# Optimization experiments

Hardware: AMD Instinct MI355X
Metric: run time of the kernel (lower is better)

## Reference

```python
import jax, jax.numpy as jnp
import numpy as np

DIM = 8   # dim == degree, required for the pol[n] * kron_power broadcast to be valid
DEG = 8
NEU = 4


def setup_inputs() -> dict:
    key = jax.random.key(0)
    ks = jax.random.split(key, DEG + 2)
    inp = {
        "X": jax.random.uniform(ks[0], (NEU, DIM), dtype=jnp.float32),      # stacked neurons
        "bias": jax.random.uniform(ks[1], (DIM,), dtype=jnp.float32),       # pol[0] for each polynomial
    }
    for n in range(1, DEG + 1):
        # pol[n] for each of the DIM polynomials: (DIM, DIM**n)
        inp[f"c{n}"] = jax.random.uniform(ks[1 + n], (DIM, DIM ** n), dtype=jnp.float32)
    return inp


def reference(X, bias, c1, c2, c3, c4, c5, c6, c7, c8):
    # output[n_idx, p_idx] = bias[p_idx] + sum_{n=1..DEG} <c_n[p_idx], kron^n(x_{n_idx})>
    coefs = [c1, c2, c3, c4, c5, c6, c7, c8]
    N = X.shape[0]
    out = jnp.broadcast_to(bias[None, :], (N, bias.shape[0]))
    K = X  # Kronecker power 1 of each neuron, shape (N, DIM)
    for i, c in enumerate(coefs):
        out = out + K @ c.T  # (N, DIM**n) @ (DIM**n, DIM) -> (N, DIM)
        if i < len(coefs) - 1:
            # khart([x, K]) == kron(x, K) per row: result[i*len(K)+j] = x[i]*K[j]
            K = (X[:, :, None] * K[:, None, :]).reshape(N, -1)
    return out
```

## Files before the change

### kernel.cpp

```cpp
#include <hip/hip_runtime.h>
#include <hip/hip_bf16.h>
#include <stdint.h>

#define OFF7 32768
#define OFF6 36864
#define OFF5 37376
#define OFF4 37440
#define NSEG 37448
#define NQ   (NSEG * 4)

typedef __attribute__((address_space(1))) const uint32_t g_u32;
typedef __attribute__((address_space(3))) uint32_t l_u32;

__device__ __forceinline__ void gload_lds16(const float* g, float* l) {
    __builtin_amdgcn_global_load_lds((g_u32*)g, (l_u32*)l, 16, 0, 0);
}

__device__ __forceinline__ float4 mul4(float4 a, float4 b) {
    return make_float4(a.x * b.x, a.y * b.y, a.z * b.z, a.w * b.w);
}
__device__ __forceinline__ float4 fma4s(float s, float4 b, float4 c) {
    return make_float4(fmaf(s, b.x, c.x), fmaf(s, b.y, c.y),
                       fmaf(s, b.z, c.z), fmaf(s, b.w, c.w));
}
__device__ __forceinline__ float4 fma44(float4 a, float4 b, float4 c) {
    return make_float4(fmaf(a.x, b.x, c.x), fmaf(a.y, b.y, c.y),
                       fmaf(a.z, b.z, c.z), fmaf(a.w, b.w, c.w));
}

struct SegInfo {
    const float* seg;
    float4 th;
    int p;
};

__device__ __forceinline__ SegInfo seg_decode(
    int g,
    const float* c4, const float* c5, const float* c6,
    const float* c7, const float* c8,
    const float4* T1s, const float4* T2s)
{
    SegInfo si;
    if (g < OFF7) {
        si.p = g >> 12; int hi = g & 4095;
        si.seg = c8 + ((size_t)si.p << 24) + ((size_t)hi << 12);
        si.th = mul4(T2s[hi >> 6], T2s[hi & 63]);
    } else if (g < OFF6) {
        int t = g - OFF7; si.p = t >> 9; int hi = t & 511;
        si.seg = c7 + ((size_t)si.p << 21) + ((size_t)hi << 12);
        si.th = mul4(T1s[hi >> 6], T2s[hi & 63]);
    } else if (g < OFF5) {
        int t = g - OFF6; si.p = t >> 6; int hi = t & 63;
        si.seg = c6 + ((size_t)si.p << 18) + ((size_t)hi << 12);
        si.th = T2s[hi];
    } else if (g < OFF4) {
        int t = g - OFF5; si.p = t >> 3; int hi = t & 7;
        si.seg = c5 + ((size_t)si.p << 15) + ((size_t)hi << 12);
        si.th = T1s[hi];
    } else {
        si.p = g - OFF4;
        si.seg = c4 + ((size_t)si.p << 12);
        si.th = make_float4(1.f, 1.f, 1.f, 1.f);
    }
    return si;
}

#define STAGE(dst, segptr, u) { \
    _Pragma("unroll") \
    for (int j_ = 0; j_ < 4; ++j_) { \
        gload_lds16((segptr) + ((((u) << 2) + j_) << 8) + (lane << 2), \
                    (dst) + (j_ << 8)); \
    } }

__global__ __launch_bounds__(256) void poly_big(
    const float* __restrict__ X,
    const float* __restrict__ c4, const float* __restrict__ c5,
    const float* __restrict__ c6, const float* __restrict__ c7,
    const float* __restrict__ c8, float* __restrict__ ws)
{
    __shared__ float4 T1s[8], T2s[64];
    __shared__ float part[32];
    __shared__ float buf[2][4096];
    const int tid = threadIdx.x;

    if (tid < 8)  T1s[tid] = make_float4(X[tid], X[8 + tid], X[16 + tid], X[24 + tid]);
    if (tid < 32) part[tid] = 0.f;
    __syncthreads();
    if (tid < 64) T2s[tid] = mul4(T1s[tid >> 3], T1s[tid & 7]);
    __syncthreads();

    const int wave = tid >> 6;
    const int lane = tid & 63;
    const int lhi  = lane >> 4;
    const float4 tl0 = T2s[((lane & 15) << 2) + 0];
    const float4 tl1 = T2s[((lane & 15) << 2) + 1];
    const float4 tl2 = T2s[((lane & 15) << 2) + 2];
    const float4 tl3 = T2s[((lane & 15) << 2) + 3];

    const int wg = (blockIdx.x << 2) + wave;
    const int NW = gridDim.x << 2;
    int Q    = (int)(((long long)wg * NQ) / NW);
    int Qend = (int)(((long long)(wg + 1) * NQ) / NW);

    if (Q < Qend) {
        float* h0 = &buf[0][wave << 10];
        float* h1 = &buf[1][wave << 10];
        float* cbuf = h0;
        float* nbuf = h1;

        SegInfo cur = seg_decode(Q >> 2, c4, c5, c6, c7, c8, T1s, T2s);
        int curu = Q & 3;
        int curp = cur.p;
        STAGE(cbuf, cur.seg, curu);

        float4 runacc = make_float4(0.f, 0.f, 0.f, 0.f);
        for (;;) {
            const bool more = (Q + 1) < Qend;
            SegInfo nxt = cur;
            int nxtu = curu;
            if (more) {
                nxtu = (Q + 1) & 3;
                nxt = seg_decode((Q + 1) >> 2, c4, c5, c6, c7, c8, T1s, T2s);
                STAGE(nbuf, nxt.seg, nxtu);
                asm volatile("s_waitcnt vmcnt(4)" ::: "memory");
            } else {
                asm volatile("s_waitcnt vmcnt(0)" ::: "memory");
            }

            float4 acc = make_float4(0.f, 0.f, 0.f, 0.f);
            #pragma unroll
            for (int q = 0; q < 4; ++q) {
                const float4 cv = *(const float4*)&cbuf[(q << 8) + (lane << 2)];
                const float4 th = T2s[(curu << 4) + (q << 2) + lhi];
                float4 inner = make_float4(cv.x * tl0.x, cv.x * tl0.y,
                                           cv.x * tl0.z, cv.x * tl0.w);
                inner = fma4s(cv.y, tl1, inner);
                inner = fma4s(cv.z, tl2, inner);
                inner = fma4s(cv.w, tl3, inner);
                acc = fma44(th, inner, acc);
            }
            runacc = fma44(acc, cur.th, runacc);

            if (!more || nxt.p != curp) {
                float vx = runacc.x, vy = runacc.y, vz = runacc.z, vw = runacc.w;
                #pragma unroll
                for (int m = 32; m; m >>= 1) {
                    vx += __shfl_xor(vx, m);
                    vy += __shfl_xor(vy, m);
                    vz += __shfl_xor(vz, m);
                    vw += __shfl_xor(vw, m);
                }
                if (lane == 0) {
                    atomicAdd(&part[(curp << 2) + 0], vx);
                    atomicAdd(&part[(curp << 2) + 1], vy);
                    atomicAdd(&part[(curp << 2) + 2], vz);
                    atomicAdd(&part[(curp << 2) + 3], vw);
                }
                runacc = make_float4(0.f, 0.f, 0.f, 0.f);
                curp = nxt.p;
            }
            if (!more) break;
            cur = nxt; curu = nxtu; ++Q;
            float* t_ = cbuf; cbuf = nbuf; nbuf = t_;
        }
    }
    __syncthreads();
    if (tid < 32) ws[(size_t)blockIdx.x * 32 + tid] = part[((tid & 7) << 2) + (tid >> 3)];
}

__global__ __launch_bounds__(1024) void poly_final(
    const float* __restrict__ X, const float* __restrict__ bias,
    const float* __restrict__ c1, const float* __restrict__ c2,
    const float* __restrict__ c3, const float* __restrict__ ws,
    int nblocks, float* __restrict__ out)
{
    __shared__ float xs[4][8];
    __shared__ float redA[32][32];
    __shared__ float redB[8][32][4];
    const int t = threadIdx.x;
    if (t < 32) xs[t >> 3][t & 7] = X[t];
    __syncthreads();

    {
        int o = t & 31, grp = t >> 5;
        float s = 0.f;
        for (int b = grp; b < nblocks; b += 32) s += ws[(size_t)b * 32 + o];
        redA[grp][o] = s;
    }
    if (t < 256) {
        int p = t >> 5, li = t & 31;
        float s0 = 0.f, s1 = 0.f, s2 = 0.f, s3 = 0.f;
        for (int i = li; i < 512; i += 32) {
            float cv = c3[(p << 9) + i];
            int d1 = (i >> 6) & 7, d2 = (i >> 3) & 7, d3 = i & 7;
            s0 = fmaf(cv, xs[0][d1] * xs[0][d2] * xs[0][d3], s0);
            s1 = fmaf(cv, xs[1][d1] * xs[1][d2] * xs[1][d3], s1);
            s2 = fmaf(cv, xs[2][d1] * xs[2][d2] * xs[2][d3], s2);
            s3 = fmaf(cv, xs[3][d1] * xs[3][d2] * xs[3][d3], s3);
        }
        for (int i = li; i < 64; i += 32) {
            float cv = c2[(p << 6) + i];
            int d1 = (i >> 3) & 7, d2 = i & 7;
            s0 = fmaf(cv, xs[0][d1] * xs[0][d2], s0);
            s1 = fmaf(cv, xs[1][d1] * xs[1][d2], s1);
            s2 = fmaf(cv, xs[2][d1] * xs[2][d2], s2);
            s3 = fmaf(cv, xs[3][d1] * xs[3][d2], s3);
        }
        if (li < 8) {
            float cv = c1[(p << 3) + li];
            s0 = fmaf(cv, xs[0][li], s0);
            s1 = fmaf(cv, xs[1][li], s1);
            s2 = fmaf(cv, xs[2][li], s2);
            s3 = fmaf(cv, xs[3][li], s3);
        }
        redB[p][li][0] = s0; redB[p][li][1] = s1; redB[p][li][2] = s2; redB[p][li][3] = s3;
    }
    __syncthreads();
    if (t < 32) {
        int neu = t >> 3, p = t & 7;
        float tot = bias[p];
        #pragma unroll
        for (int grp = 0; grp < 32; ++grp) tot += redA[grp][t];
        for (int li = 0; li < 32; ++li) tot += redB[p][li][neu];
        out[t] = tot;
    }
}

extern "C" void kernel_launch(void* const* d_in, const int* in_sizes, int n_in,
                              void* d_out, int out_size, void* d_ws, size_t ws_size,
                              hipStream_t stream) {
    const float* X    = (const float*)d_in[0];
    const float* bias = (const float*)d_in[1];
    const float* c1   = (const float*)d_in[2];
    const float* c2   = (const float*)d_in[3];
    const float* c3   = (const float*)d_in[4];
    const float* c4   = (const float*)d_in[5];
    const float* c5   = (const float*)d_in[6];
    const float* c6   = (const float*)d_in[7];
    const float* c7   = (const float*)d_in[8];
    const float* c8   = (const float*)d_in[9];
    float* out = (float*)d_out;
    float* ws  = (float*)d_ws;

    int blocks = 1024;
    size_t maxb = ws_size / (32 * sizeof(float));
    if ((size_t)blocks > maxb) blocks = (int)maxb;
    if (blocks < 1) blocks = 1;

    poly_big<<<blocks, 256, 0, stream>>>(X, c4, c5, c6, c7, c8, ws);
    poly_final<<<1, 1024, 0, stream>>>(X, bias, c1, c2, c3, ws, blocks, out);
}
```

Baseline: 130.0 us.

## Replace workspace reduction with global atomics and interleave wave quad assignment

```diff
diff --git a/kernel.cpp b/kernel.cpp
--- a/kernel.cpp
+++ b/kernel.cpp
@@ -76,15 +76,13 @@
     const float* __restrict__ X,
     const float* __restrict__ c4, const float* __restrict__ c5,
     const float* __restrict__ c6, const float* __restrict__ c7,
-    const float* __restrict__ c8, float* __restrict__ ws)
+    const float* __restrict__ c8, float* __restrict__ out)
 {
     __shared__ float4 T1s[8], T2s[64];
-    __shared__ float part[32];
     __shared__ float buf[2][4096];
     const int tid = threadIdx.x;
 
     if (tid < 8)  T1s[tid] = make_float4(X[tid], X[8 + tid], X[16 + tid], X[24 + tid]);
-    if (tid < 32) part[tid] = 0.f;
     __syncthreads();
     if (tid < 64) T2s[tid] = mul4(T1s[tid >> 3], T1s[tid & 7]);
     __syncthreads();
@@ -97,30 +95,31 @@
     const float4 tl2 = T2s[((lane & 15) << 2) + 2];
     const float4 tl3 = T2s[((lane & 15) << 2) + 3];
 
-    const int wg = (blockIdx.x << 2) + wave;
-    const int NW = gridDim.x << 2;
-    int Q    = (int)(((long long)wg * NQ) / NW);
-    int Qend = (int)(((long long)(wg + 1) * NQ) / NW);
-
-    if (Q < Qend) {
-        float* h0 = &buf[0][wave << 10];
-        float* h1 = &buf[1][wave << 10];
-        float* cbuf = h0;
-        float* nbuf = h1;
-
-        SegInfo cur = seg_decode(Q >> 2, c4, c5, c6, c7, c8, T1s, T2s);
-        int curu = Q & 3;
+    const int nB = gridDim.x;
+    const int Qb   = (int)(((long long)blockIdx.x * NQ) / nB);
+    const int nloc = (int)(((long long)(blockIdx.x + 1) * NQ) / nB) - Qb;
+
+    int i = wave;
+    if (i < nloc) {
+        float* cbuf = &buf[0][wave << 10];
+        float* nbuf = &buf[1][wave << 10];
+
+        int Qg = Qb + i;
+        SegInfo cur = seg_decode(Qg >> 2, c4, c5, c6, c7, c8, T1s, T2s);
+        int curu = Qg & 3;
         int curp = cur.p;
         STAGE(cbuf, cur.seg, curu);
 
         float4 runacc = make_float4(0.f, 0.f, 0.f, 0.f);
         for (;;) {
-            const bool more = (Q + 1) < Qend;
+            const int inext = i + 4;
+            const bool more = inext < nloc;
             SegInfo nxt = cur;
             int nxtu = curu;
             if (more) {
-                nxtu = (Q + 1) & 3;
-                nxt = seg_decode((Q + 1) >> 2, c4, c5, c6, c7, c8, T1s, T2s);
+                const int Qn = Qb + inext;
+                nxtu = Qn & 3;
+                nxt = seg_decode(Qn >> 2, c4, c5, c6, c7, c8, T1s, T2s);
                 STAGE(nbuf, nxt.seg, nxtu);
                 asm volatile("s_waitcnt vmcnt(4)" ::: "memory");
             } else {
@@ -151,78 +150,69 @@
                     vw += __shfl_xor(vw, m);
                 }
                 if (lane == 0) {
-                    atomicAdd(&part[(curp << 2) + 0], vx);
-                    atomicAdd(&part[(curp << 2) + 1], vy);
-                    atomicAdd(&part[(curp << 2) + 2], vz);
-                    atomicAdd(&part[(curp << 2) + 3], vw);
+                    atomicAdd(&out[ 0 + curp], vx);
+                    atomicAdd(&out[ 8 + curp], vy);
+                    atomicAdd(&out[16 + curp], vz);
+                    atomicAdd(&out[24 + curp], vw);
                 }
                 runacc = make_float4(0.f, 0.f, 0.f, 0.f);
                 curp = nxt.p;
             }
             if (!more) break;
-            cur = nxt; curu = nxtu; ++Q;
             float* t_ = cbuf; cbuf = nbuf; nbuf = t_;
+            cur = nxt; curu = nxtu; i = inext;
         }
     }
-    __syncthreads();
-    if (tid < 32) ws[(size_t)blockIdx.x * 32 + tid] = part[((tid & 7) << 2) + (tid >> 3)];
-}
-
-__global__ __launch_bounds__(1024) void poly_final(
+}
+
+__global__ __launch_bounds__(256) void poly_small(
     const float* __restrict__ X, const float* __restrict__ bias,
     const float* __restrict__ c1, const float* __restrict__ c2,
-    const float* __restrict__ c3, const float* __restrict__ ws,
-    int nblocks, float* __restrict__ out)
+    const float* __restrict__ c3, float* __restrict__ out)
 {
     __shared__ float xs[4][8];
-    __shared__ float redA[32][32];
-    __shared__ float redB[8][32][4];
     const int t = threadIdx.x;
     if (t < 32) xs[t >> 3][t & 7] = X[t];
     __syncthreads();
 
-    {
-        int o = t & 31, grp = t >> 5;
-        float s = 0.f;
-        for (int b = grp; b < nblocks; b += 32) s += ws[(size_t)b * 32 + o];
-        redA[grp][o] = s;
-    }
-    if (t < 256) {
-        int p = t >> 5, li = t & 31;
-        float s0 = 0.f, s1 = 0.f, s2 = 0.f, s3 = 0.f;
-        for (int i = li; i < 512; i += 32) {
-            float cv = c3[(p << 9) + i];
-            int d1 = (i >> 6) & 7, d2 = (i >> 3) & 7, d3 = i & 7;
-            s0 = fmaf(cv, xs[0][d1] * xs[0][d2] * xs[0][d3], s0);
-            s1 = fmaf(cv, xs[1][d1] * xs[1][d2] * xs[1][d3], s1);
-            s2 = fmaf(cv, xs[2][d1] * xs[2][d2] * xs[2][d3], s2);
-            s3 = fmaf(cv, xs[3][d1] * xs[3][d2] * xs[3][d3], s3);
-        }
-        for (int i = li; i < 64; i += 32) {
-            float cv = c2[(p << 6) + i];
-            int d1 = (i >> 3) & 7, d2 = i & 7;
-            s0 = fmaf(cv, xs[0][d1] * xs[0][d2], s0);
-            s1 = fmaf(cv, xs[1][d1] * xs[1][d2], s1);
-            s2 = fmaf(cv, xs[2][d1] * xs[2][d2], s2);
-            s3 = fmaf(cv, xs[3][d1] * xs[3][d2], s3);
-        }
-        if (li < 8) {
-            float cv = c1[(p << 3) + li];
-            s0 = fmaf(cv, xs[0][li], s0);
-            s1 = fmaf(cv, xs[1][li], s1);
-            s2 = fmaf(cv, xs[2][li], s2);
-            s3 = fmaf(cv, xs[3][li], s3);
-        }
-        redB[p][li][0] = s0; redB[p][li][1] = s1; redB[p][li][2] = s2; redB[p][li][3] = s3;
-    }
-    __syncthreads();
-    if (t < 32) {
-        int neu = t >> 3, p = t & 7;
-        float tot = bias[p];
-        #pragma unroll
-        for (int grp = 0; grp < 32; ++grp) tot += redA[grp][t];
-        for (int li = 0; li < 32; ++li) tot += redB[p][li][neu];
-        out[t] = tot;
+    const int p = t >> 5, li = t & 31;
+    float s0 = 0.f, s1 = 0.f, s2 = 0.f, s3 = 0.f;
+    for (int i = li; i < 512; i += 32) {
+        float cv = c3[(p << 9) + i];
+        int d1 = (i >> 6) & 7, d2 = (i >> 3) & 7, d3 = i & 7;
+        s0 = fmaf(cv, xs[0][d1] * xs[0][d2] * xs[0][d3], s0);
+        s1 = fmaf(cv, xs[1][d1] * xs[1][d2] * xs[1][d3], s1);
+        s2 = fmaf(cv, xs[2][d1] * xs[2][d2] * xs[2][d3], s2);
+        s3 = fmaf(cv, xs[3][d1] * xs[3][d2] * xs[3][d3], s3);
+    }
+    for (int i = li; i < 64; i += 32) {
+        float cv = c2[(p << 6) + i];
+        int d1 = (i >> 3) & 7, d2 = i & 7;
+        s0 = fmaf(cv, xs[0][d1] * xs[0][d2], s0);
+        s1 = fmaf(cv, xs[1][d1] * xs[1][d2], s1);
+        s2 = fmaf(cv, xs[2][d1] * xs[2][d2], s2);
+        s3 = fmaf(cv, xs[3][d1] * xs[3][d2], s3);
+    }
+    if (li < 8) {
+        float cv = c1[(p << 3) + li];
+        s0 = fmaf(cv, xs[0][li], s0);
+        s1 = fmaf(cv, xs[1][li], s1);
+        s2 = fmaf(cv, xs[2][li], s2);
+        s3 = fmaf(cv, xs[3][li], s3);
+    }
+    #pragma unroll
+    for (int m = 16; m; m >>= 1) {
+        s0 += __shfl_xor(s0, m);
+        s1 += __shfl_xor(s1, m);
+        s2 += __shfl_xor(s2, m);
+        s3 += __shfl_xor(s3, m);
+    }
+    if (li == 0) {
+        const float b = bias[p];
+        out[ 0 + p] = b + s0;
+        out[ 8 + p] = b + s1;
+        out[16 + p] = b + s2;
+        out[24 + p] = b + s3;
     }
 }
 
@@ -240,13 +230,7 @@
     const float* c7   = (const float*)d_in[8];
     const float* c8   = (const float*)d_in[9];
     float* out = (float*)d_out;
-    float* ws  = (float*)d_ws;
-
-    int blocks = 1024;
-    size_t maxb = ws_size / (32 * sizeof(float));
-    if ((size_t)blocks > maxb) blocks = (int)maxb;
-    if (blocks < 1) blocks = 1;
-
-    poly_big<<<blocks, 256, 0, stream>>>(X, c4, c5, c6, c7, c8, ws);
-    poly_final<<<1, 1024, 0, stream>>>(X, bias, c1, c2, c3, ws, blocks, out);
-}
+
+    poly_small<<<1, 256, 0, stream>>>(X, bias, c1, c2, c3, out);
+    poly_big<<<1024, 256, 0, stream>>>(X, c4, c5, c6, c7, c8, out);
+}
```

Measured after the change: 203.1 us. +56.3%, slower.
